# Performance work log

Hardware: AMD Instinct MI355X
Metric: run time of the kernel (lower is better)

## Reference

```python
import jax, jax.numpy as jnp
import numpy as np

N = 40000   # num nodes (== in_channels, featureless RGCN)
E = 640000  # num edges
R = 8       # num relations
H = 128     # hidden channels
C = 64      # out channels


def setup_inputs() -> dict:
    key = jax.random.key(0)
    k = jax.random.split(key, 8)
    edge_index = jax.random.randint(k[0], (2, E), 0, N)
    edge_type = jax.random.randint(k[1], (E,), 0, R)
    s1 = 1.0 / np.sqrt(N)
    s2 = 1.0 / np.sqrt(H)
    W1 = jax.random.normal(k[2], (R, N, H), jnp.float32) * s1
    root1 = jax.random.normal(k[3], (N, H), jnp.float32) * s1
    b1 = jnp.zeros((H,), jnp.float32)
    W2 = jax.random.normal(k[4], (R, H, C), jnp.float32) * s2
    root2 = jax.random.normal(k[5], (H, C), jnp.float32) * s2
    b2 = jnp.zeros((C,), jnp.float32)
    return {"edge_index": edge_index, "edge_type": edge_type,
            "W1": W1, "root1": root1, "b1": b1,
            "W2": W2, "root2": root2, "b2": b2}


def _segment_mean_per_relation(msg, dst, etype, n_nodes, n_rel):
    # mean aggregation per (destination node, relation), then sum over relations
    seg = dst * n_rel + etype                      # [E]
    sums = jax.ops.segment_sum(msg, seg, num_segments=n_nodes * n_rel)
    cnt = jax.ops.segment_sum(jnp.ones((msg.shape[0], 1), msg.dtype), seg,
                              num_segments=n_nodes * n_rel)
    mean = sums / jnp.maximum(cnt, 1.0)            # [N*R, F]
    return mean.reshape(n_nodes, n_rel, -1).sum(axis=1)  # [N, F]


def reference(edge_index, edge_type, W1, root1, b1, W2, root2, b2):
    src, dst = edge_index[0], edge_index[1]
    # ---- conv1 (x=None): message = W1[rel] row of the source node ----
    msg1 = W1[edge_type, src]                      # [E, H] gather
    h = _segment_mean_per_relation(msg1, dst, edge_type, N, R)
    h = h + root1 + b1                             # root weight acts as embedding
    h = jax.nn.relu(h)
    # ---- conv2: per-relation dense transform then gather per edge ----
    h_all = jnp.einsum('nh,rhc->rnc', h, W2)       # [R, N, C]
    msg2 = h_all[edge_type, src]                   # [E, C]
    out = _segment_mean_per_relation(msg2, dst, edge_type, N, R)
    out = out + h @ root2 + b2                     # [N, C]
    return out
```

## Files before the change

### kernel.cpp

```cpp
#include <hip/hip_runtime.h>

#define N_NODES 40000
#define N_EDGES 640000
#define N_REL   8
#define H_DIM   128
#define C_DIM   64
#define NR      (N_NODES * N_REL)
#define SCAN_NB ((NR + 1023) / 1024)

typedef __attribute__((ext_vector_type(8))) short bf16x8;
typedef __attribute__((ext_vector_type(4))) float f32x4;

__device__ inline uint rne_bf16(float x) {
    uint u = __float_as_uint(x);
    return (u + 0x7FFFu + ((u >> 16) & 1u)) >> 16;
}
__device__ inline uint pack_bf16(float x, float y) {
    return rne_bf16(x) | (rne_bf16(y) << 16);
}
__device__ inline float bf_lo(uint v) { return __uint_as_float(v << 16); }
__device__ inline float bf_hi(uint v) { return __uint_as_float(v & 0xFFFF0000u); }

__global__ void count_rank(const int* __restrict__ ei, const int* __restrict__ et,
                           int* __restrict__ cnt, int* __restrict__ rank) {
    int e = blockIdx.x * blockDim.x + threadIdx.x;
    if (e < N_EDGES) {
        int seg = ei[N_EDGES + e] * N_REL + et[e];
        rank[e] = atomicAdd(&cnt[seg], 1);
    }
}

__global__ void scanA(const int* __restrict__ cnt, int* __restrict__ segbase,
                      int* __restrict__ bsum) {
    __shared__ int lds[256];
    int base = blockIdx.x * 1024;
    int t = threadIdx.x;
    int v[4]; int s = 0;
    #pragma unroll
    for (int j = 0; j < 4; j++) {
        int idx = base + t * 4 + j;
        v[j] = (idx < NR) ? cnt[idx] : 0;
        s += v[j];
    }
    lds[t] = s; __syncthreads();
    int x = s;
    #pragma unroll
    for (int off = 1; off < 256; off <<= 1) {
        int y = (t >= off) ? lds[t - off] : 0;
        __syncthreads();
        x += y; lds[t] = x;
        __syncthreads();
    }
    int excl = x - s;
    #pragma unroll
    for (int j = 0; j < 4; j++) {
        int idx = base + t * 4 + j;
        if (idx < NR) segbase[idx] = excl;
        excl += v[j];
    }
    if (t == 255) bsum[blockIdx.x] = x;
}

__global__ __launch_bounds__(512) void
scanB(int* __restrict__ bsum, int* __restrict__ segbase) {
    __shared__ int lds[512];
    int t = threadIdx.x;
    int v = (t < SCAN_NB) ? bsum[t] : 0;
    lds[t] = v; __syncthreads();
    int x = v;
    for (int off = 1; off < 512; off <<= 1) {
        int y = (t >= off) ? lds[t - off] : 0;
        __syncthreads();
        x += y; lds[t] = x;
        __syncthreads();
    }
    if (t < SCAN_NB) bsum[t] = x - v;
    if (t == 511) segbase[NR] = x;
}

__global__ void scanC(int* __restrict__ segbase, const int* __restrict__ bsum) {
    int idx = blockIdx.x * blockDim.x + threadIdx.x;
    if (idx < NR) segbase[idx] += bsum[idx >> 10];
}

__global__ void scatter_kernel(const int* __restrict__ ei, const int* __restrict__ et,
                               const int* __restrict__ segbase, const int* __restrict__ cnt,
                               const int* __restrict__ rank, int2* __restrict__ em) {
    int e = blockIdx.x * blockDim.x + threadIdx.x;
    if (e < N_EDGES) {
        int r = et[e];
        int seg = ei[N_EDGES + e] * N_REL + r;
        int o = segbase[seg] + rank[e];
        em[o] = make_int2(ei[e] | (r << 16),
                          __float_as_int(1.0f / (float)cnt[seg]));
    }
}

__global__ void convert_w2(const float* __restrict__ W2, const float* __restrict__ root2,
                           ushort* __restrict__ w2t) {
    int i = blockIdx.x * 256 + threadIdx.x;
    if (i >= 9 * C_DIM * H_DIM) return;
    int k = i & 127; int c = (i >> 7) & 63; int r = i >> 13;
    float v = (r < 8) ? W2[((size_t)r * H_DIM + k) * C_DIM + c]
                      : root2[(size_t)k * C_DIM + c];
    int byte = (c * 256 + k * 2) ^ ((c & 7) << 4);
    w2t[(size_t)r * 8192 + (byte >> 1)] = (ushort)rne_bf16(v);
}

__global__ __launch_bounds__(256) void
conv1_gather(const int2* __restrict__ em, const int* __restrict__ segbase,
             const float* __restrict__ W1, const float* __restrict__ root1,
             const float* __restrict__ b1, uint* __restrict__ h16) {
    int lane = threadIdx.x & 63, wv = threadIdx.x >> 6;
    int eg = lane >> 5, q = lane & 31;
    int n = blockIdx.x * 4 + wv;
    int e0 = segbase[n * N_REL], e1 = segbase[n * N_REL + N_REL];
    float4 acc = make_float4(0.f, 0.f, 0.f, 0.f);
    for (int base = e0; base < e1; base += 64) {
        int m = e1 - base; if (m > 64) m = 64;
        int2 md = make_int2(0, 0);
        if (lane < m) md = em[base + lane];
        int i = 0;
        for (; i + 8 <= m; i += 8) {
            int i0 = i + eg, i1 = i + eg + 2, i2 = i + eg + 4, i3 = i + eg + 6;
            int p0 = __shfl(md.x, i0), p1 = __shfl(md.x, i1);
            int p2 = __shfl(md.x, i2), p3 = __shfl(md.x, i3);
            float w0 = __int_as_float(__shfl(md.y, i0));
            float w1 = __int_as_float(__shfl(md.y, i1));
            float w2 = __int_as_float(__shfl(md.y, i2));
            float w3 = __int_as_float(__shfl(md.y, i3));
            float4 v0 = ((const float4*)(W1 + ((size_t)(p0 >> 16) * N_NODES + (p0 & 0xFFFF)) * H_DIM))[q];
            float4 v1 = ((const float4*)(W1 + ((size_t)(p1 >> 16) * N_NODES + (p1 & 0xFFFF)) * H_DIM))[q];
            float4 v2 = ((const float4*)(W1 + ((size_t)(p2 >> 16) * N_NODES + (p2 & 0xFFFF)) * H_DIM))[q];
            float4 v3 = ((const float4*)(W1 + ((size_t)(p3 >> 16) * N_NODES + (p3 & 0xFFFF)) * H_DIM))[q];
            acc.x += w0 * v0.x + w1 * v1.x + w2 * v2.x + w3 * v3.x;
            acc.y += w0 * v0.y + w1 * v1.y + w2 * v2.y + w3 * v3.y;
            acc.z += w0 * v0.z + w1 * v1.z + w2 * v2.z + w3 * v3.z;
            acc.w += w0 * v0.w + w1 * v1.w + w2 * v2.w + w3 * v3.w;
        }
        for (; i < m; i += 2) {
            int ii = i + eg;
            int srcl = (ii < m) ? ii : 0;
            int p = __shfl(md.x, srcl);
            float w = __int_as_float(__shfl(md.y, srcl));
            if (ii < m) {
                float4 v = ((const float4*)(W1 + ((size_t)(p >> 16) * N_NODES + (p & 0xFFFF)) * H_DIM))[q];
                acc.x += w * v.x; acc.y += w * v.y;
                acc.z += w * v.z; acc.w += w * v.w;
            }
        }
    }
    acc.x += __shfl_xor(acc.x, 32);
    acc.y += __shfl_xor(acc.y, 32);
    acc.z += __shfl_xor(acc.z, 32);
    acc.w += __shfl_xor(acc.w, 32);
    if (eg == 0) {
        float4 rt = ((const float4*)root1)[(size_t)n * 32 + q];
        float4 bb = ((const float4*)b1)[q];
        float cx = fmaxf(acc.x + rt.x + bb.x, 0.f);
        float cy = fmaxf(acc.y + rt.y + bb.y, 0.f);
        float cz = fmaxf(acc.z + rt.z + bb.z, 0.f);
        float cw = fmaxf(acc.w + rt.w + bb.w, 0.f);
        uint2 o; o.x = pack_bf16(cx, cy); o.y = pack_bf16(cz, cw);
        ((uint2*)h16)[(size_t)n * 32 + q] = o;
    }
}

__global__ __launch_bounds__(256) void
zgemm(const uint* __restrict__ h16, const ushort* __restrict__ w2t,
      const float* __restrict__ b2, ushort* __restrict__ zb, float* __restrict__ out) {
    __shared__ uint ldsA[4096];
    __shared__ uint ldsB[4096];
    int t = threadIdx.x, lane = t & 63, wv = t >> 6;
    int nbase = blockIdx.x * 64;
    for (int i = t; i < 4096; i += 256) {
        int row = i >> 6, cu = i & 63;
        int byte = (row * 256 + cu * 4) ^ ((row & 7) << 4);
        ldsA[byte >> 2] = h16[(size_t)(nbase + row) * 64 + cu];
    }
    const char* pA = (const char*)ldsA;
    const char* pB = (const char*)ldsB;
    int arow = wv * 16 + (lane & 15);
    int qk = (lane >> 4) * 16;
    for (int rr = 0; rr < 9; rr++) {
        __syncthreads();
        const uint4* bsrc = (const uint4*)(w2t + (size_t)rr * 8192);
        ((uint4*)ldsB)[t]       = bsrc[t];
        ((uint4*)ldsB)[t + 256] = bsrc[t + 256];
        ((uint4*)ldsB)[t + 512] = bsrc[t + 512];
        ((uint4*)ldsB)[t + 768] = bsrc[t + 768];
        __syncthreads();
        f32x4 acc[4];
        #pragma unroll
        for (int ct = 0; ct < 4; ct++) acc[ct] = (f32x4){0.f, 0.f, 0.f, 0.f};
        #pragma unroll
        for (int ct = 0; ct < 4; ct++) {
            int bcol = ct * 16 + (lane & 15);
            #pragma unroll
            for (int kf = 0; kf < 4; kf++) {
                int abyte = (arow * 256 + kf * 64 + qk) ^ ((arow & 7) << 4);
                int bbyte = (bcol * 256 + kf * 64 + qk) ^ ((bcol & 7) << 4);
                bf16x8 a = *(const bf16x8*)(pA + abyte);
                bf16x8 b = *(const bf16x8*)(pB + bbyte);
                acc[ct] = __builtin_amdgcn_mfma_f32_16x16x32_bf16(a, b, acc[ct], 0, 0, 0);
            }
        }
        #pragma unroll
        for (int ct = 0; ct < 4; ct++) {
            int c = ct * 16 + (lane & 15);
            #pragma unroll
            for (int j = 0; j < 4; j++) {
                int n = nbase + wv * 16 + (lane >> 4) * 4 + j;
                if (rr < 8)
                    zb[((size_t)rr * N_NODES + n) * 64 + c] = (ushort)rne_bf16(acc[ct][j]);
                else
                    out[(size_t)n * 64 + c] = acc[ct][j] + b2[c];
            }
        }
    }
}

__global__ __launch_bounds__(256) void
zgather(const int2* __restrict__ em, const int* __restrict__ segbase,
        const uint* __restrict__ zb32, float* __restrict__ out) {
    int lane = threadIdx.x & 63, wv = threadIdx.x >> 6;
    int n = blockIdx.x * 4 + wv;
    int eg = lane >> 5, c2 = lane & 31;
    int e0 = segbase[n * N_REL], e1 = segbase[n * N_REL + N_REL];
    float ax = 0.f, ay = 0.f;
    for (int base = e0; base < e1; base += 64) {
        int m = e1 - base; if (m > 64) m = 64;
        int2 md = make_int2(0, 0);
        if (lane < m) md = em[base + lane];
        int i = 0;
        for (; i + 16 <= m; i += 16) {
            #pragma unroll
            for (int u = 0; u < 2; u++) {
                int j0 = i + u * 8 + eg, j1 = j0 + 2, j2 = j0 + 4, j3 = j0 + 6;
                int p0 = __shfl(md.x, j0), p1 = __shfl(md.x, j1);
                int p2 = __shfl(md.x, j2), p3 = __shfl(md.x, j3);
                float w0 = __int_as_float(__shfl(md.y, j0));
                float w1 = __int_as_float(__shfl(md.y, j1));
                float w2 = __int_as_float(__shfl(md.y, j2));
                float w3 = __int_as_float(__shfl(md.y, j3));
                uint z0 = zb32[((size_t)(p0 >> 16) * N_NODES + (p0 & 0xFFFF)) * 32 + c2];
                uint z1 = zb32[((size_t)(p1 >> 16) * N_NODES + (p1 & 0xFFFF)) * 32 + c2];
                uint z2 = zb32[((size_t)(p2 >> 16) * N_NODES + (p2 & 0xFFFF)) * 32 + c2];
                uint z3 = zb32[((size_t)(p3 >> 16) * N_NODES + (p3 & 0xFFFF)) * 32 + c2];
                ax += w0 * bf_lo(z0) + w1 * bf_lo(z1) + w2 * bf_lo(z2) + w3 * bf_lo(z3);
                ay += w0 * bf_hi(z0) + w1 * bf_hi(z1) + w2 * bf_hi(z2) + w3 * bf_hi(z3);
            }
        }
        for (; i + 8 <= m; i += 8) {
            int j0 = i + eg, j1 = j0 + 2, j2 = j0 + 4, j3 = j0 + 6;
            int p0 = __shfl(md.x, j0), p1 = __shfl(md.x, j1);
            int p2 = __shfl(md.x, j2), p3 = __shfl(md.x, j3);
            float w0 = __int_as_float(__shfl(md.y, j0));
            float w1 = __int_as_float(__shfl(md.y, j1));
            float w2 = __int_as_float(__shfl(md.y, j2));
            float w3 = __int_as_float(__shfl(md.y, j3));
            uint z0 = zb32[((size_t)(p0 >> 16) * N_NODES + (p0 & 0xFFFF)) * 32 + c2];
            uint z1 = zb32[((size_t)(p1 >> 16) * N_NODES + (p1 & 0xFFFF)) * 32 + c2];
            uint z2 = zb32[((size_t)(p2 >> 16) * N_NODES + (p2 & 0xFFFF)) * 32 + c2];
            uint z3 = zb32[((size_t)(p3 >> 16) * N_NODES + (p3 & 0xFFFF)) * 32 + c2];
            ax += w0 * bf_lo(z0) + w1 * bf_lo(z1) + w2 * bf_lo(z2) + w3 * bf_lo(z3);
            ay += w0 * bf_hi(z0) + w1 * bf_hi(z1) + w2 * bf_hi(z2) + w3 * bf_hi(z3);
        }
        for (; i < m; i += 2) {
            int ii = i + eg;
            int srcl = (ii < m) ? ii : 0;
            int p = __shfl(md.x, srcl);
            float w = __int_as_float(__shfl(md.y, srcl));
            if (ii < m) {
                uint zv = zb32[((size_t)(p >> 16) * N_NODES + (p & 0xFFFF)) * 32 + c2];
                ax += w * bf_lo(zv);
                ay += w * bf_hi(zv);
            }
        }
    }
    ax += __shfl_xor(ax, 32);
    ay += __shfl_xor(ay, 32);
    if (eg == 0) {
        float2* o = (float2*)out + (size_t)n * 32 + c2;
        float2 v = *o;
        v.x += ax; v.y += ay;
        *o = v;
    }
}

extern "C" void kernel_launch(void* const* d_in, const int* in_sizes, int n_in,
                              void* d_out, int out_size, void* d_ws, size_t ws_size,
                              hipStream_t stream) {
    const int*   ei    = (const int*)d_in[0];
    const int*   et    = (const int*)d_in[1];
    const float* W1    = (const float*)d_in[2];
    const float* root1 = (const float*)d_in[3];
    const float* b1    = (const float*)d_in[4];
    const float* W2    = (const float*)d_in[5];
    const float* root2 = (const float*)d_in[6];
    const float* b2    = (const float*)d_in[7];
    float* out = (float*)d_out;

    int*    cnt     = (int*)d_ws;
    int*    segbase = cnt + NR;
    int*    bsum    = segbase + NR + 16;
    int*    rank    = bsum + 512;
    int2*   em      = (int2*)(rank + N_EDGES);
    uint*   h16     = (uint*)(em + N_EDGES);
    ushort* w2t     = (ushort*)(h16 + (size_t)N_NODES * 64);
    ushort* zb      = w2t + 9 * 8192;

    hipMemsetAsync(cnt, 0, (size_t)NR * sizeof(int), stream);

    count_rank    <<<(N_EDGES + 255) / 256, 256, 0, stream>>>(ei, et, cnt, rank);
    convert_w2    <<<(9 * C_DIM * H_DIM + 255) / 256, 256, 0, stream>>>(W2, root2, w2t);
    scanA         <<<SCAN_NB, 256, 0, stream>>>(cnt, segbase, bsum);
    scanB         <<<1, 512, 0, stream>>>(bsum, segbase);
    scanC         <<<(NR + 255) / 256, 256, 0, stream>>>(segbase, bsum);
    scatter_kernel<<<(N_EDGES + 255) / 256, 256, 0, stream>>>(ei, et, segbase, cnt, rank, em);
    conv1_gather  <<<N_NODES / 4, 256, 0, stream>>>(em, segbase, W1, root1, b1, h16);
    zgemm         <<<N_NODES / 64, 256, 0, stream>>>(h16, w2t, b2, zb, out);
    zgather       <<<N_NODES / 4, 256, 0, stream>>>(em, segbase, (const uint*)zb, out);
}
```

Before: 369.6 us.

## Gather bf16 copy of W1, compact edge metadata, fuse conversion with counting

W1 is converted to bf16 on every call, and conv1 then gathers 256-byte rows instead of 512-byte fp32 rows. The conversion runs inside the same launch as edge counting and the W2 conversion. Edge metadata shrinks from int2 to a single int. The per-(node, relation) mean weight is now computed from counts inside the gather kernels and fetched by lane shuffle, instead of being stored per edge. The aim is to halve the random-gather traffic in conv1. In exchange, each call pays a full streaming read and write over the 164 MB W1 table, and conv1 accumulates from bf16 inputs, which loses precision.

```diff
diff --git a/kernel.cpp b/kernel.cpp
--- a/kernel.cpp
+++ b/kernel.cpp
@@ -7,6 +7,9 @@
 #define C_DIM   64
 #define NR      (N_NODES * N_REL)
 #define SCAN_NB ((NR + 1023) / 1024)
+#define EDGE_NB  (N_EDGES / 256)
+#define W1CVT_NB ((N_REL * N_NODES * H_DIM / 4) / 256)
+#define W2CVT_NB (9 * C_DIM * H_DIM / 256)
 
 typedef __attribute__((ext_vector_type(8))) short bf16x8;
 typedef __attribute__((ext_vector_type(4))) float f32x4;
@@ -21,12 +24,29 @@
 __device__ inline float bf_lo(uint v) { return __uint_as_float(v << 16); }
 __device__ inline float bf_hi(uint v) { return __uint_as_float(v & 0xFFFF0000u); }
 
-__global__ void count_rank(const int* __restrict__ ei, const int* __restrict__ et,
-                           int* __restrict__ cnt, int* __restrict__ rank) {
-    int e = blockIdx.x * blockDim.x + threadIdx.x;
-    if (e < N_EDGES) {
+__global__ __launch_bounds__(256) void
+build_convert(const int* __restrict__ ei, const int* __restrict__ et,
+              int* __restrict__ cnt, int* __restrict__ rank,
+              const float* __restrict__ W1, ushort* __restrict__ w1b,
+              const float* __restrict__ W2, const float* __restrict__ root2,
+              ushort* __restrict__ w2t) {
+    int b = blockIdx.x, t = threadIdx.x;
+    if (b < EDGE_NB) {
+        int e = b * 256 + t;
         int seg = ei[N_EDGES + e] * N_REL + et[e];
         rank[e] = atomicAdd(&cnt[seg], 1);
+    } else if (b < EDGE_NB + W1CVT_NB) {
+        long i = (long)(b - EDGE_NB) * 256 + t;
+        float4 v = ((const float4*)W1)[i];
+        uint2 o; o.x = pack_bf16(v.x, v.y); o.y = pack_bf16(v.z, v.w);
+        ((uint2*)w1b)[i] = o;
+    } else {
+        int i = (b - EDGE_NB - W1CVT_NB) * 256 + t;
+        int k = i & 127; int c = (i >> 7) & 63; int r = i >> 13;
+        float v = (r < 8) ? W2[((size_t)r * H_DIM + k) * C_DIM + c]
+                          : root2[(size_t)k * C_DIM + c];
+        int byte = (c * 256 + k * 2) ^ ((c & 7) << 4);
+        w2t[(size_t)r * 8192 + (byte >> 1)] = (ushort)rne_bf16(v);
     }
 }
 
@@ -84,69 +104,58 @@
 }
 
 __global__ void scatter_kernel(const int* __restrict__ ei, const int* __restrict__ et,
-                               const int* __restrict__ segbase, const int* __restrict__ cnt,
-                               const int* __restrict__ rank, int2* __restrict__ em) {
+                               const int* __restrict__ segbase,
+                               const int* __restrict__ rank, int* __restrict__ em) {
     int e = blockIdx.x * blockDim.x + threadIdx.x;
     if (e < N_EDGES) {
         int r = et[e];
         int seg = ei[N_EDGES + e] * N_REL + r;
-        int o = segbase[seg] + rank[e];
-        em[o] = make_int2(ei[e] | (r << 16),
-                          __float_as_int(1.0f / (float)cnt[seg]));
-    }
-}
-
-__global__ void convert_w2(const float* __restrict__ W2, const float* __restrict__ root2,
-                           ushort* __restrict__ w2t) {
-    int i = blockIdx.x * 256 + threadIdx.x;
-    if (i >= 9 * C_DIM * H_DIM) return;
-    int k = i & 127; int c = (i >> 7) & 63; int r = i >> 13;
-    float v = (r < 8) ? W2[((size_t)r * H_DIM + k) * C_DIM + c]
-                      : root2[(size_t)k * C_DIM + c];
-    int byte = (c * 256 + k * 2) ^ ((c & 7) << 4);
-    w2t[(size_t)r * 8192 + (byte >> 1)] = (ushort)rne_bf16(v);
+        em[segbase[seg] + rank[e]] = ei[e] | (r << 16);
+    }
 }
 
 __global__ __launch_bounds__(256) void
-conv1_gather(const int2* __restrict__ em, const int* __restrict__ segbase,
-             const float* __restrict__ W1, const float* __restrict__ root1,
-             const float* __restrict__ b1, uint* __restrict__ h16) {
+conv1_gather(const int* __restrict__ em, const int* __restrict__ segbase,
+             const int* __restrict__ cnt, const ushort* __restrict__ w1b,
+             const float* __restrict__ root1, const float* __restrict__ b1,
+             uint* __restrict__ h16) {
     int lane = threadIdx.x & 63, wv = threadIdx.x >> 6;
     int eg = lane >> 5, q = lane & 31;
     int n = blockIdx.x * 4 + wv;
     int e0 = segbase[n * N_REL], e1 = segbase[n * N_REL + N_REL];
+    int c = (lane < N_REL) ? cnt[n * N_REL + lane] : 1;
+    float invreg = 1.0f / (float)((c > 0) ? c : 1);
     float4 acc = make_float4(0.f, 0.f, 0.f, 0.f);
     for (int base = e0; base < e1; base += 64) {
         int m = e1 - base; if (m > 64) m = 64;
-        int2 md = make_int2(0, 0);
-        if (lane < m) md = em[base + lane];
+        int md = (lane < m) ? em[base + lane] : 0;
         int i = 0;
         for (; i + 8 <= m; i += 8) {
-            int i0 = i + eg, i1 = i + eg + 2, i2 = i + eg + 4, i3 = i + eg + 6;
-            int p0 = __shfl(md.x, i0), p1 = __shfl(md.x, i1);
-            int p2 = __shfl(md.x, i2), p3 = __shfl(md.x, i3);
-            float w0 = __int_as_float(__shfl(md.y, i0));
-            float w1 = __int_as_float(__shfl(md.y, i1));
-            float w2 = __int_as_float(__shfl(md.y, i2));
-            float w3 = __int_as_float(__shfl(md.y, i3));
-            float4 v0 = ((const float4*)(W1 + ((size_t)(p0 >> 16) * N_NODES + (p0 & 0xFFFF)) * H_DIM))[q];
-            float4 v1 = ((const float4*)(W1 + ((size_t)(p1 >> 16) * N_NODES + (p1 & 0xFFFF)) * H_DIM))[q];
-            float4 v2 = ((const float4*)(W1 + ((size_t)(p2 >> 16) * N_NODES + (p2 & 0xFFFF)) * H_DIM))[q];
-            float4 v3 = ((const float4*)(W1 + ((size_t)(p3 >> 16) * N_NODES + (p3 & 0xFFFF)) * H_DIM))[q];
-            acc.x += w0 * v0.x + w1 * v1.x + w2 * v2.x + w3 * v3.x;
-            acc.y += w0 * v0.y + w1 * v1.y + w2 * v2.y + w3 * v3.y;
-            acc.z += w0 * v0.z + w1 * v1.z + w2 * v2.z + w3 * v3.z;
-            acc.w += w0 * v0.w + w1 * v1.w + w2 * v2.w + w3 * v3.w;
+            int i0 = i + eg, i1 = i0 + 2, i2 = i0 + 4, i3 = i0 + 6;
+            int p0 = __shfl(md, i0), p1 = __shfl(md, i1);
+            int p2 = __shfl(md, i2), p3 = __shfl(md, i3);
+            float w0 = __shfl(invreg, p0 >> 16);
+            float w1 = __shfl(invreg, p1 >> 16);
+            float w2 = __shfl(invreg, p2 >> 16);
+            float w3 = __shfl(invreg, p3 >> 16);
+            uint2 v0 = ((const uint2*)(w1b + ((size_t)(p0 >> 16) * N_NODES + (p0 & 0xFFFF)) * H_DIM))[q];
+            uint2 v1 = ((const uint2*)(w1b + ((size_t)(p1 >> 16) * N_NODES + (p1 & 0xFFFF)) * H_DIM))[q];
+            uint2 v2 = ((const uint2*)(w1b + ((size_t)(p2 >> 16) * N_NODES + (p2 & 0xFFFF)) * H_DIM))[q];
+            uint2 v3 = ((const uint2*)(w1b + ((size_t)(p3 >> 16) * N_NODES + (p3 & 0xFFFF)) * H_DIM))[q];
+            acc.x += w0 * bf_lo(v0.x) + w1 * bf_lo(v1.x) + w2 * bf_lo(v2.x) + w3 * bf_lo(v3.x);
+            acc.y += w0 * bf_hi(v0.x) + w1 * bf_hi(v1.x) + w2 * bf_hi(v2.x) + w3 * bf_hi(v3.x);
+            acc.z += w0 * bf_lo(v0.y) + w1 * bf_lo(v1.y) + w2 * bf_lo(v2.y) + w3 * bf_lo(v3.y);
+            acc.w += w0 * bf_hi(v0.y) + w1 * bf_hi(v1.y) + w2 * bf_hi(v2.y) + w3 * bf_hi(v3.y);
         }
         for (; i < m; i += 2) {
             int ii = i + eg;
             int srcl = (ii < m) ? ii : 0;
-            int p = __shfl(md.x, srcl);
-            float w = __int_as_float(__shfl(md.y, srcl));
+            int p = __shfl(md, srcl);
+            float w = __shfl(invreg, p >> 16);
             if (ii < m) {
-                float4 v = ((const float4*)(W1 + ((size_t)(p >> 16) * N_NODES + (p & 0xFFFF)) * H_DIM))[q];
-                acc.x += w * v.x; acc.y += w * v.y;
-                acc.z += w * v.z; acc.w += w * v.w;
+                uint2 v = ((const uint2*)(w1b + ((size_t)(p >> 16) * N_NODES + (p & 0xFFFF)) * H_DIM))[q];
+                acc.x += w * bf_lo(v.x); acc.y += w * bf_hi(v.x);
+                acc.z += w * bf_lo(v.y); acc.w += w * bf_hi(v.y);
             }
         }
     }
@@ -221,28 +230,30 @@
 }
 
 __global__ __launch_bounds__(256) void
-zgather(const int2* __restrict__ em, const int* __restrict__ segbase,
-        const uint* __restrict__ zb32, float* __restrict__ out) {
+zgather(const int* __restrict__ em, const int* __restrict__ segbase,
+        const int* __restrict__ cnt, const uint* __restrict__ zb32,
+        float* __restrict__ out) {
     int lane = threadIdx.x & 63, wv = threadIdx.x >> 6;
     int n = blockIdx.x * 4 + wv;
     int eg = lane >> 5, c2 = lane & 31;
     int e0 = segbase[n * N_REL], e1 = segbase[n * N_REL + N_REL];
+    int c = (lane < N_REL) ? cnt[n * N_REL + lane] : 1;
+    float invreg = 1.0f / (float)((c > 0) ? c : 1);
     float ax = 0.f, ay = 0.f;
     for (int base = e0; base < e1; base += 64) {
         int m = e1 - base; if (m > 64) m = 64;
-        int2 md = make_int2(0, 0);
-        if (lane < m) md = em[base + lane];
+        int md = (lane < m) ? em[base + lane] : 0;
         int i = 0;
         for (; i + 16 <= m; i += 16) {
             #pragma unroll
             for (int u = 0; u < 2; u++) {
                 int j0 = i + u * 8 + eg, j1 = j0 + 2, j2 = j0 + 4, j3 = j0 + 6;
-                int p0 = __shfl(md.x, j0), p1 = __shfl(md.x, j1);
-                int p2 = __shfl(md.x, j2), p3 = __shfl(md.x, j3);
-                float w0 = __int_as_float(__shfl(md.y, j0));
-                float w1 = __int_as_float(__shfl(md.y, j1));
-                float w2 = __int_as_float(__shfl(md.y, j2));
-                float w3 = __int_as_float(__shfl(md.y, j3));
+                int p0 = __shfl(md, j0), p1 = __shfl(md, j1);
+                int p2 = __shfl(md, j2), p3 = __shfl(md, j3);
+                float w0 = __shfl(invreg, p0 >> 16);
+                float w1 = __shfl(invreg, p1 >> 16);
+                float w2 = __shfl(invreg, p2 >> 16);
+                float w3 = __shfl(invreg, p3 >> 16);
                 uint z0 = zb32[((size_t)(p0 >> 16) * N_NODES + (p0 & 0xFFFF)) * 32 + c2];
                 uint z1 = zb32[((size_t)(p1 >> 16) * N_NODES + (p1 & 0xFFFF)) * 32 + c2];
                 uint z2 = zb32[((size_t)(p2 >> 16) * N_NODES + (p2 & 0xFFFF)) * 32 + c2];
@@ -253,12 +264,12 @@
         }
         for (; i + 8 <= m; i += 8) {
             int j0 = i + eg, j1 = j0 + 2, j2 = j0 + 4, j3 = j0 + 6;
-            int p0 = __shfl(md.x, j0), p1 = __shfl(md.x, j1);
-            int p2 = __shfl(md.x, j2), p3 = __shfl(md.x, j3);
-            float w0 = __int_as_float(__shfl(md.y, j0));
-            float w1 = __int_as_float(__shfl(md.y, j1));
-            float w2 = __int_as_float(__shfl(md.y, j2));
-            float w3 = __int_as_float(__shfl(md.y, j3));
+            int p0 = __shfl(md, j0), p1 = __shfl(md, j1);
+            int p2 = __shfl(md, j2), p3 = __shfl(md, j3);
+            float w0 = __shfl(invreg, p0 >> 16);
+            float w1 = __shfl(invreg, p1 >> 16);
+            float w2 = __shfl(invreg, p2 >> 16);
+            float w3 = __shfl(invreg, p3 >> 16);
             uint z0 = zb32[((size_t)(p0 >> 16) * N_NODES + (p0 & 0xFFFF)) * 32 + c2];
             uint z1 = zb32[((size_t)(p1 >> 16) * N_NODES + (p1 & 0xFFFF)) * 32 + c2];
             uint z2 = zb32[((size_t)(p2 >> 16) * N_NODES + (p2 & 0xFFFF)) * 32 + c2];
@@ -269,8 +280,8 @@
         for (; i < m; i += 2) {
             int ii = i + eg;
             int srcl = (ii < m) ? ii : 0;
-            int p = __shfl(md.x, srcl);
-            float w = __int_as_float(__shfl(md.y, srcl));
+            int p = __shfl(md, srcl);
+            float w = __shfl(invreg, p >> 16);
             if (ii < m) {
                 uint zv = zb32[((size_t)(p >> 16) * N_NODES + (p & 0xFFFF)) * 32 + c2];
                 ax += w * bf_lo(zv);
@@ -305,20 +316,21 @@
     int*    segbase = cnt + NR;
     int*    bsum    = segbase + NR + 16;
     int*    rank    = bsum + 512;
-    int2*   em      = (int2*)(rank + N_EDGES);
+    int*    em      = rank + N_EDGES;
     uint*   h16     = (uint*)(em + N_EDGES);
     ushort* w2t     = (ushort*)(h16 + (size_t)N_NODES * 64);
-    ushort* zb      = w2t + 9 * 8192;
+    ushort* w1b     = w2t + 9 * 8192;
+    ushort* zb      = w1b + (size_t)N_REL * N_NODES * H_DIM;
 
     hipMemsetAsync(cnt, 0, (size_t)NR * sizeof(int), stream);
 
-    count_rank    <<<(N_EDGES + 255) / 256, 256, 0, stream>>>(ei, et, cnt, rank);
-    convert_w2    <<<(9 * C_DIM * H_DIM + 255) / 256, 256, 0, stream>>>(W2, root2, w2t);
+    build_convert <<<EDGE_NB + W1CVT_NB + W2CVT_NB, 256, 0, stream>>>(
+                      ei, et, cnt, rank, W1, w1b, W2, root2, w2t);
     scanA         <<<SCAN_NB, 256, 0, stream>>>(cnt, segbase, bsum);
     scanB         <<<1, 512, 0, stream>>>(bsum, segbase);
     scanC         <<<(NR + 255) / 256, 256, 0, stream>>>(segbase, bsum);
-    scatter_kernel<<<(N_EDGES + 255) / 256, 256, 0, stream>>>(ei, et, segbase, cnt, rank, em);
-    conv1_gather  <<<N_NODES / 4, 256, 0, stream>>>(em, segbase, W1, root1, b1, h16);
+    scatter_kernel<<<(N_EDGES + 255) / 256, 256, 0, stream>>>(ei, et, segbase, rank, em);
+    conv1_gather  <<<N_NODES / 4, 256, 0, stream>>>(em, segbase, cnt, w1b, root1, b1, h16);
     zgemm         <<<N_NODES / 64, 256, 0, stream>>>(h16, w2t, b2, zb, out);
-    zgather       <<<N_NODES / 4, 256, 0, stream>>>(em, segbase, (const uint*)zb, out);
-}
+    zgather       <<<N_NODES / 4, 256, 0, stream>>>(em, segbase, cnt, (const uint*)zb, out);
+}
```

Measured after the change: 389.2 us. 1.05x slower.
